# Kernel tuning notes

Measured on AMD Instinct MI355X. Metric: run time of the kernel, lower is better.

Reference implementation:

```python
import jax, jax.numpy as jnp
import numpy as np

N = 8192
IN_DIM = 64
OUT_DIM = 64
HEADS = 2
EPS = 1e-10


def setup_inputs() -> dict:
    key = jax.random.key(0)
    ks = jax.random.split(key, 6)
    features = jax.random.normal(ks[0], (N, IN_DIM), dtype=jnp.float32)
    adj = (jax.random.uniform(ks[1], (N, N)) < 0.005).astype(jnp.float32)
    # per-head attention linear: Linear(2*in_dim, 1) stacked -> [heads, 2*in_dim]
    W_attn = jax.random.normal(ks[2], (HEADS, 2 * IN_DIM), dtype=jnp.float32) * 0.05
    b_attn = jax.random.normal(ks[3], (HEADS,), dtype=jnp.float32) * 0.05
    # feature transform: Linear(in_dim, heads*out_dim)
    W_lin = jax.random.normal(ks[4], (HEADS * OUT_DIM, IN_DIM), dtype=jnp.float32) * 0.05
    b_lin = jax.random.normal(ks[5], (HEADS * OUT_DIM,), dtype=jnp.float32) * 0.05
    return {"adj": adj, "features": features, "W_attn": W_attn,
            "b_attn": b_attn, "W_lin": W_lin, "b_lin": b_lin}


def reference(adj, features, W_attn, b_attn, W_lin, b_lin):
    n, in_dim = features.shape
    heads = W_attn.shape[0]
    # add self-loops (adj + sparse identity in the original)
    idx = jnp.arange(n)
    adj_sl = adj.at[idx, idx].add(1.0)
    # concat-based score: head([x_i ; x_j]) = x_i @ Wa_src + x_j @ Wa_dst + b
    # (avoids the O(N^2 * 2*in_dim) concat tensor the original materializes)
    s_src = features @ W_attn[:, :in_dim].T   # [N, H]
    s_dst = features @ W_attn[:, in_dim:].T   # [N, H]
    # scores[n,h,m] = exp(s_src[n,h] + s_dst[m,h] + b[h])
    scores = jnp.exp(s_src[:, :, None] + s_dst.T[None, :, :] + b_attn[None, :, None])
    scores = scores * adj_sl[:, None, :]                      # adjacency mask
    attn = scores / (jnp.sum(scores, axis=-1, keepdims=True) + EPS)
    # dropout is identity in eval mode (deterministic reference)
    ft = (features @ W_lin.T + b_lin).reshape(n, heads, -1)   # [N, H, OUT]
    out = jnp.einsum('nhm,mhj->nhj', attn, ft)                # aggregate neighbors
    return jax.nn.elu(out.reshape(n, -1))
```

## Files before the change

kernel.cpp:

```cpp
#include <hip/hip_runtime.h>
#include <math.h>

#define NN 8192
#define IN_DIM 64
#define GAT_EPS 1e-10f
#define ECAP 256

typedef float fvec4 __attribute__((ext_vector_type(4)));

__device__ __forceinline__ unsigned nz4(fvec4 v) {
    return (unsigned)(v.x != 0.f) | ((unsigned)(v.y != 0.f) << 1) |
           ((unsigned)(v.z != 0.f) << 2) | ((unsigned)(v.w != 0.f) << 3);
}

__global__ void ft_kernel(const float* __restrict__ features,
                          const float* __restrict__ W_lin,
                          const float* __restrict__ b_lin,
                          float2* __restrict__ ftI) {
    int gid = blockIdx.x * blockDim.x + threadIdx.x;
    int n = gid >> 6;
    int c = gid & 63;
    const float4* f4 = (const float4*)(features + (size_t)n * IN_DIM);
    const float4* w0 = (const float4*)(W_lin + (size_t)c * IN_DIM);
    const float4* w1 = (const float4*)(W_lin + (size_t)(64 + c) * IN_DIM);
    float a0 = 0.f, a1 = 0.f;
#pragma unroll
    for (int d = 0; d < IN_DIM / 4; ++d) {
        float4 f = f4[d];
        float4 u = w0[d];
        float4 v = w1[d];
        a0 += f.x * u.x + f.y * u.y + f.z * u.z + f.w * u.w;
        a1 += f.x * v.x + f.y * v.y + f.z * v.z + f.w * v.w;
    }
    ftI[gid] = make_float2(a0 + b_lin[c], a1 + b_lin[64 + c]);
}

__global__ void score_kernel(const float* __restrict__ features,
                             const float* __restrict__ W_attn,
                             float2* __restrict__ pdv) {
    int n = blockIdx.x * blockDim.x + threadIdx.x;
    const float4* f4   = (const float4*)(features + (size_t)n * IN_DIM);
    const float4* wa0d = (const float4*)(W_attn + IN_DIM);
    const float4* wa1d = (const float4*)(W_attn + 3 * IN_DIM);
    float s0 = 0.f, s1 = 0.f;
#pragma unroll
    for (int d = 0; d < IN_DIM / 4; ++d) {
        float4 f = f4[d];
        float4 b = wa0d[d];
        float4 e = wa1d[d];
        s0 += f.x * b.x + f.y * b.y + f.z * b.z + f.w * b.w;
        s1 += f.x * e.x + f.y * e.y + f.z * e.z + f.w * e.w;
    }
    pdv[n] = make_float2(__expf(s0), __expf(s1));
}

__global__ void __launch_bounds__(256) gat_agg_kernel(
        const float* __restrict__ adj,
        const float2* __restrict__ ftI,
        const float2* __restrict__ pdv,
        float* __restrict__ out) {
    __shared__ int edges[4][ECAP];
    __shared__ int ecnt[4];
    int widx = threadIdx.x >> 6;
    int lane = threadIdx.x & 63;
    int n = blockIdx.x * 4 + widx;
    int* ebuf = edges[widx];

    if (lane == 0) ecnt[widx] = 0;

    const fvec4* arow = (const fvec4*)(adj + (size_t)n * NN) + lane;

    fvec4 a0 = __builtin_nontemporal_load(arow);
    fvec4 a1 = __builtin_nontemporal_load(arow + 64);
    fvec4 a2 = __builtin_nontemporal_load(arow + 128);
    fvec4 a3 = __builtin_nontemporal_load(arow + 192);

#pragma unroll
    for (int it = 0; it < 8; ++it) {
        fvec4 b0, b1, b2, b3;
        if (it < 7) {
            const fvec4* p = arow + (it + 1) * 256;
            b0 = __builtin_nontemporal_load(p);
            b1 = __builtin_nontemporal_load(p + 64);
            b2 = __builtin_nontemporal_load(p + 128);
            b3 = __builtin_nontemporal_load(p + 192);
        }
        unsigned mb = nz4(a0) | (nz4(a1) << 4) | (nz4(a2) << 8) | (nz4(a3) << 12);
        if (mb) {
            int c = __popc(mb);
            int pos = atomicAdd(&ecnt[widx], c);
            int megabase = it * 1024 + lane * 4;
            while (mb) {
                int b = __ffs(mb) - 1;
                mb &= mb - 1;
                ebuf[pos++] = megabase + ((b >> 2) << 8) + (b & 3);
            }
        }
        a0 = b0; a1 = b1; a2 = b2; a3 = b3;
    }

    float2 ps = pdv[n];
    float2 fs = ftI[(size_t)n * 64 + lane];
    float acc0 = ps.x * fs.x, acc1 = ps.y * fs.y;
    float den0 = ps.x, den1 = ps.y;

    __syncthreads();

    int count = ecnt[widx];
    int e = 0;
    for (; e + 8 <= count; e += 8) {
        int4 ma  = *(const int4*)&ebuf[e];
        int4 mbq = *(const int4*)&ebuf[e + 4];
        float2 p0 = pdv[ma.x],  p1 = pdv[ma.y],  p2 = pdv[ma.z],  p3 = pdv[ma.w];
        float2 p4 = pdv[mbq.x], p5 = pdv[mbq.y], p6 = pdv[mbq.z], p7 = pdv[mbq.w];
        float2 f0 = ftI[(size_t)ma.x * 64 + lane];
        float2 f1 = ftI[(size_t)ma.y * 64 + lane];
        float2 f2 = ftI[(size_t)ma.z * 64 + lane];
        float2 f3 = ftI[(size_t)ma.w * 64 + lane];
        float2 f4 = ftI[(size_t)mbq.x * 64 + lane];
        float2 f5 = ftI[(size_t)mbq.y * 64 + lane];
        float2 f6 = ftI[(size_t)mbq.z * 64 + lane];
        float2 f7 = ftI[(size_t)mbq.w * 64 + lane];
        acc0 += p0.x * f0.x + p1.x * f1.x + p2.x * f2.x + p3.x * f3.x
              + p4.x * f4.x + p5.x * f5.x + p6.x * f6.x + p7.x * f7.x;
        acc1 += p0.y * f0.y + p1.y * f1.y + p2.y * f2.y + p3.y * f3.y
              + p4.y * f4.y + p5.y * f5.y + p6.y * f6.y + p7.y * f7.y;
        den0 += p0.x + p1.x + p2.x + p3.x + p4.x + p5.x + p6.x + p7.x;
        den1 += p0.y + p1.y + p2.y + p3.y + p4.y + p5.y + p6.y + p7.y;
    }
    for (; e < count; ++e) {
        int m = ebuf[e];
        float2 p = pdv[m];
        float2 f = ftI[(size_t)m * 64 + lane];
        acc0 += p.x * f.x;
        acc1 += p.y * f.y;
        den0 += p.x;
        den1 += p.y;
    }

    float o0 = acc0 / (den0 + GAT_EPS);
    float o1 = acc1 / (den1 + GAT_EPS);
    o0 = o0 > 0.f ? o0 : expm1f(o0);
    o1 = o1 > 0.f ? o1 : expm1f(o1);
    out[(size_t)n * 128 + lane]      = o0;
    out[(size_t)n * 128 + 64 + lane] = o1;
}

extern "C" void kernel_launch(void* const* d_in, const int* in_sizes, int n_in,
                              void* d_out, int out_size, void* d_ws, size_t ws_size,
                              hipStream_t stream) {
    const float* adj      = (const float*)d_in[0];
    const float* features = (const float*)d_in[1];
    const float* W_attn   = (const float*)d_in[2];
    const float* W_lin    = (const float*)d_in[4];
    const float* b_lin    = (const float*)d_in[5];
    float* out = (float*)d_out;

    float* ws = (float*)d_ws;
    float2* ftI = (float2*)ws;
    float2* pdv = (float2*)(ws + (size_t)NN * 128);

    ft_kernel<<<(NN * 64) / 256, 256, 0, stream>>>(features, W_lin, b_lin, ftI);
    score_kernel<<<NN / 256, 256, 0, stream>>>(features, W_attn, pdv);
    gat_agg_kernel<<<NN / 4, 256, 0, stream>>>(adj, ftI, pdv, out);
}
```

Measured before the change: 398.3 us.

## Merge setup kernels and deepen adjacency prefetch to three stages

Merges the feature-transform and score kernels into one launch, with block ranges picking the branch, which removes one kernel launch and its gap. In the aggregation kernel, the adjacency row stream changes from double buffering to a three-slot rotating prefetch, so two chunks of loads are in flight while one is scanned. The adjacency scan is bandwidth-bound, and the deeper prefetch is meant to keep more memory requests outstanding. The cost is higher register use, which may lower occupancy.

```diff
diff --git a/kernel.cpp b/kernel.cpp
--- a/kernel.cpp
+++ b/kernel.cpp
@@ -13,45 +13,45 @@
            ((unsigned)(v.z != 0.f) << 2) | ((unsigned)(v.w != 0.f) << 3);
 }
 
-__global__ void ft_kernel(const float* __restrict__ features,
-                          const float* __restrict__ W_lin,
-                          const float* __restrict__ b_lin,
-                          float2* __restrict__ ftI) {
-    int gid = blockIdx.x * blockDim.x + threadIdx.x;
-    int n = gid >> 6;
-    int c = gid & 63;
-    const float4* f4 = (const float4*)(features + (size_t)n * IN_DIM);
-    const float4* w0 = (const float4*)(W_lin + (size_t)c * IN_DIM);
-    const float4* w1 = (const float4*)(W_lin + (size_t)(64 + c) * IN_DIM);
-    float a0 = 0.f, a1 = 0.f;
+__global__ void setup_kernel(const float* __restrict__ features,
+                             const float* __restrict__ W_lin,
+                             const float* __restrict__ b_lin,
+                             const float* __restrict__ W_attn,
+                             float2* __restrict__ ftI,
+                             float2* __restrict__ pdv) {
+    if (blockIdx.x < 2048) {
+        int gid = blockIdx.x * blockDim.x + threadIdx.x;
+        int n = gid >> 6;
+        int c = gid & 63;
+        const float4* f4 = (const float4*)(features + (size_t)n * IN_DIM);
+        const float4* w0 = (const float4*)(W_lin + (size_t)c * IN_DIM);
+        const float4* w1 = (const float4*)(W_lin + (size_t)(64 + c) * IN_DIM);
+        float a0 = 0.f, a1 = 0.f;
 #pragma unroll
-    for (int d = 0; d < IN_DIM / 4; ++d) {
-        float4 f = f4[d];
-        float4 u = w0[d];
-        float4 v = w1[d];
-        a0 += f.x * u.x + f.y * u.y + f.z * u.z + f.w * u.w;
-        a1 += f.x * v.x + f.y * v.y + f.z * v.z + f.w * v.w;
+        for (int d = 0; d < IN_DIM / 4; ++d) {
+            float4 f = f4[d];
+            float4 u = w0[d];
+            float4 v = w1[d];
+            a0 += f.x * u.x + f.y * u.y + f.z * u.z + f.w * u.w;
+            a1 += f.x * v.x + f.y * v.y + f.z * v.z + f.w * v.w;
+        }
+        ftI[gid] = make_float2(a0 + b_lin[c], a1 + b_lin[64 + c]);
+    } else {
+        int n = (blockIdx.x - 2048) * blockDim.x + threadIdx.x;
+        const float4* f4   = (const float4*)(features + (size_t)n * IN_DIM);
+        const float4* wa0d = (const float4*)(W_attn + IN_DIM);
+        const float4* wa1d = (const float4*)(W_attn + 3 * IN_DIM);
+        float s0 = 0.f, s1 = 0.f;
+#pragma unroll
+        for (int d = 0; d < IN_DIM / 4; ++d) {
+            float4 f = f4[d];
+            float4 b = wa0d[d];
+            float4 e = wa1d[d];
+            s0 += f.x * b.x + f.y * b.y + f.z * b.z + f.w * b.w;
+            s1 += f.x * e.x + f.y * e.y + f.z * e.z + f.w * e.w;
+        }
+        pdv[n] = make_float2(__expf(s0), __expf(s1));
     }
-    ftI[gid] = make_float2(a0 + b_lin[c], a1 + b_lin[64 + c]);
-}
-
-__global__ void score_kernel(const float* __restrict__ features,
-                             const float* __restrict__ W_attn,
-                             float2* __restrict__ pdv) {
-    int n = blockIdx.x * blockDim.x + threadIdx.x;
-    const float4* f4   = (const float4*)(features + (size_t)n * IN_DIM);
-    const float4* wa0d = (const float4*)(W_attn + IN_DIM);
-    const float4* wa1d = (const float4*)(W_attn + 3 * IN_DIM);
-    float s0 = 0.f, s1 = 0.f;
-#pragma unroll
-    for (int d = 0; d < IN_DIM / 4; ++d) {
-        float4 f = f4[d];
-        float4 b = wa0d[d];
-        float4 e = wa1d[d];
-        s0 += f.x * b.x + f.y * b.y + f.z * b.z + f.w * b.w;
-        s1 += f.x * e.x + f.y * e.y + f.z * e.z + f.w * e.w;
-    }
-    pdv[n] = make_float2(__expf(s0), __expf(s1));
 }
 
 __global__ void __launch_bounds__(256) gat_agg_kernel(
@@ -70,20 +70,26 @@
 
     const fvec4* arow = (const fvec4*)(adj + (size_t)n * NN) + lane;
 
-    fvec4 a0 = __builtin_nontemporal_load(arow);
-    fvec4 a1 = __builtin_nontemporal_load(arow + 64);
-    fvec4 a2 = __builtin_nontemporal_load(arow + 128);
-    fvec4 a3 = __builtin_nontemporal_load(arow + 192);
+    fvec4 q[3][4];
+#pragma unroll
+    for (int r = 0; r < 3; ++r) {
+        const fvec4* p = arow + r * 256;
+        q[r][0] = __builtin_nontemporal_load(p);
+        q[r][1] = __builtin_nontemporal_load(p + 64);
+        q[r][2] = __builtin_nontemporal_load(p + 128);
+        q[r][3] = __builtin_nontemporal_load(p + 192);
+    }
 
 #pragma unroll
     for (int it = 0; it < 8; ++it) {
-        fvec4 b0, b1, b2, b3;
-        if (it < 7) {
-            const fvec4* p = arow + (it + 1) * 256;
-            b0 = __builtin_nontemporal_load(p);
-            b1 = __builtin_nontemporal_load(p + 64);
-            b2 = __builtin_nontemporal_load(p + 128);
-            b3 = __builtin_nontemporal_load(p + 192);
+        int slot = it % 3;
+        fvec4 a0 = q[slot][0], a1 = q[slot][1], a2 = q[slot][2], a3 = q[slot][3];
+        if (it < 5) {
+            const fvec4* p = arow + (it + 3) * 256;
+            q[slot][0] = __builtin_nontemporal_load(p);
+            q[slot][1] = __builtin_nontemporal_load(p + 64);
+            q[slot][2] = __builtin_nontemporal_load(p + 128);
+            q[slot][3] = __builtin_nontemporal_load(p + 192);
         }
         unsigned mb = nz4(a0) | (nz4(a1) << 4) | (nz4(a2) << 8) | (nz4(a3) << 12);
         if (mb) {
@@ -96,7 +102,6 @@
                 ebuf[pos++] = megabase + ((b >> 2) << 8) + (b & 3);
             }
         }
-        a0 = b0; a1 = b1; a2 = b2; a3 = b3;
     }
 
     float2 ps = pdv[n];
@@ -160,7 +165,6 @@
     float2* ftI = (float2*)ws;
     float2* pdv = (float2*)(ws + (size_t)NN * 128);
 
-    ft_kernel<<<(NN * 64) / 256, 256, 0, stream>>>(features, W_lin, b_lin, ftI);
-    score_kernel<<<NN / 256, 256, 0, stream>>>(features, W_attn, pdv);
+    setup_kernel<<<2048 + 32, 256, 0, stream>>>(features, W_lin, b_lin, W_attn, ftI, pdv);
     gat_agg_kernel<<<NN / 4, 256, 0, stream>>>(adj, ftI, pdv, out);
 }
```

Result: no change. 391.7 us (-1.6%).
